# Performance work log

Hardware: AMD Instinct MI355X
Metric: run time of the kernel (lower is better)

The kernel has to match this reference:

```python
import jax, jax.numpy as jnp
import numpy as np
from jax import lax

# dims: batch, seq_len, d_model, heads, d_ff, num_scales, compression_ratio
B, L, D, H, F, S, CR = 4, 1024, 1024, 16, 4096, 4, 2


def setup_inputs() -> dict:
    key = jax.random.key(0)
    ks = jax.random.split(key, 12)
    def rn(k, shape, s=0.02):
        return jax.random.normal(k, shape, dtype=jnp.float32) * s
    return {
        'x': jax.random.normal(ks[0], (B, L, D), dtype=jnp.float32),
        'W_dc': rn(ks[1], (D, D, 3)),            # dilated conv kernel (OIH)
        'b_dc': jnp.zeros((D,), jnp.float32),
        'W_dec': rn(ks[2], (S - 1, D, D, CR)),    # strided decomposition convs
        'Wq': rn(ks[3], (S, D, D)),               # per-scale query proj
        'Wk': rn(ks[4], (S, D, D)),               # per-scale key proj
        'Wv': rn(ks[5], (D, D)),                  # shared value proj
        'Wo': rn(ks[6], (D, D)),                  # shared output proj
        'agg_logits': rn(ks[7], (S,), 1.0),       # convex aggregation logits
        'gamma1': jnp.ones((D,), jnp.float32), 'beta1': jnp.zeros((D,), jnp.float32),
        'gamma2': jnp.ones((D,), jnp.float32), 'beta2': jnp.zeros((D,), jnp.float32),
        'W1': rn(ks[8], (D, F)), 'b1': jnp.zeros((F,), jnp.float32),
        'W2': rn(ks[9], (F, D)), 'b2': jnp.zeros((D,), jnp.float32),
    }


def _conv1d(x_blc, w_oik, stride, pad, rdil):
    # x: [B, L, Cin] -> [B, L', Cout]; w: [Cout, Cin, K]
    y = lax.conv_general_dilated(
        x_blc.transpose(0, 2, 1), w_oik, (stride,), [(pad, pad)],
        rhs_dilation=(rdil,), dimension_numbers=('NCH', 'OIH', 'NCH'))
    return y.transpose(0, 2, 1)


def _ln(x, g, b, eps=1e-5):
    mu = x.mean(-1, keepdims=True)
    v = x.var(-1, keepdims=True)
    return (x - mu) * lax.rsqrt(v + eps) * g + b


def reference(x, W_dc, b_dc, W_dec, Wq, Wk, Wv, Wo, agg_logits,
              gamma1, beta1, gamma2, beta2, W1, b1, W2, b2):
    dh = D // H
    inv_sqrt_dh = 1.0 / jnp.sqrt(jnp.float32(dh))
    residual = x
    # 1. dilated conv (k=3, dil=2, pad=2 -> same length) + ReLU (dropout=eval/identity)
    xc = jax.nn.relu(_conv1d(x, W_dc, 1, 2, 2) + b_dc)
    # 2. hierarchical decomposition: strided convs halving seq length per scale
    scales = [xc]
    for s in range(S - 1):
        scales.append(_conv1d(scales[-1], W_dec[s], CR, 0, 1))
    # 3. multiscale attention: full-res queries attend to each compressed scale;
    #    value projection Wv shared across scales
    outs = []
    for s in range(S):
        Ls = scales[s].shape[1]
        q = (xc @ Wq[s]).reshape(B, L, H, dh)
        k = (scales[s] @ Wk[s]).reshape(B, Ls, H, dh)
        v = (scales[s] @ Wv).reshape(B, Ls, H, dh)
        att = jax.nn.softmax(jnp.einsum('bqhd,bkhd->bhqk', q, k) * inv_sqrt_dh, axis=-1)
        o = jnp.einsum('bhqk,bkhd->bqhd', att, v).reshape(B, L, D) @ Wo
        outs.append(o)
    # 4. convex (optimization-driven) aggregation + entropy sparsity aux loss
    w = jax.nn.softmax(agg_logits)
    maha = jnp.einsum('s,sbld->bld', w, jnp.stack(outs))
    aux_loss = -jnp.sum(w * jnp.log(w + 1e-9))
    # 5. residual + LN + FFN (exact GELU, as torch nn.GELU default)
    x1 = _ln(residual + maha, gamma1, beta1)
    ffn = jax.nn.gelu(x1 @ W1 + b1, approximate=False) @ W2 + b2
    out = _ln(x1 + ffn, gamma2, beta2)
    return out, aux_loss
```

## Files before the change

kernel.cpp:

```cpp
#include <hip/hip_runtime.h>
#include <cstddef>

#define DB 4
#define DL 1024
#define DD 1024
#define DH 16
#define DF 4096

typedef __attribute__((ext_vector_type(8))) short short8;
typedef __attribute__((ext_vector_type(4))) float float4v;

static __device__ __forceinline__ short f2bf(float f) {
    unsigned u = __float_as_uint(f);
    unsigned r = (u + 0x7FFFu + ((u >> 16) & 1u)) >> 16;
    return (short)r;
}

#define GLOAD_LDS16(gp, lp)                                                          \
    __builtin_amdgcn_global_load_lds(                                                \
        (const __attribute__((address_space(1))) void*)(gp),                         \
        (__attribute__((address_space(3))) void*)(lp), 16, 0, 0)

__global__ __launch_bounds__(256) void prep_all_kernel(
    const float* __restrict__ Wdc, const float* __restrict__ Wdec,
    const float* __restrict__ Wq, const float* __restrict__ Wk,
    const float* __restrict__ Wv, const float* __restrict__ Wo,
    const float* __restrict__ W1, const float* __restrict__ W2,
    const float* __restrict__ x, const float* __restrict__ agg,
    short* __restrict__ wdc_bt, short* __restrict__ wdec_bt,
    short* __restrict__ wq4t, short* __restrict__ wkvt, short* __restrict__ wot,
    short* __restrict__ w1t, short* __restrict__ w2t, short* __restrict__ xpad,
    float* __restrict__ wagg, float* __restrict__ aux) {
    __shared__ float tile[32][33];
    const size_t M1 = 1024 * 1024;
    int blk = blockIdx.x, tid = threadIdx.x;
    if (blk < 12288) {
        int idx = blk * 256 + tid;
        int i = idx & 1023, o = (idx >> 10) & 1023, k = idx >> 20;
        wdc_bt[idx] = f2bf(Wdc[((size_t)o * 1024 + i) * 3 + k]);
        return;
    }
    if (blk < 36864) {
        int idx = (blk - 12288) * 256 + tid;
        int i = idx & 1023, k2 = (idx >> 10) & 1, n = (idx >> 11) & 1023, s = idx >> 21;
        wdec_bt[idx] = f2bf(Wdec[(((size_t)(s * 1024 + n)) * 1024 + i) * 2 + k2]);
        return;
    }
    if (blk < 58368) {
        const float* src; short* dst; int K, N, bx, by;
        if (blk < 50176) {
            int r = blk - 36864;
            int z = r >> 10, rem = r & 1023;
            bx = rem & 31; by = rem >> 5; K = 1024; N = 1024;
            if (z < 4)      { src = Wq + (size_t)z * M1;       dst = wq4t + (size_t)z * M1; }
            else if (z < 8) { src = Wk + (size_t)(z - 4) * M1; dst = wkvt + (size_t)(z - 4) * 2 * M1; }
            else if (z < 12){ src = Wv;                        dst = wkvt + (size_t)(z - 8) * 2 * M1 + M1; }
            else            { src = Wo;                        dst = wot; }
        } else if (blk < 54272) {
            int r = blk - 50176;
            bx = r & 127; by = r >> 7; K = 1024; N = 4096; src = W1; dst = w1t;
        } else {
            int r = blk - 54272;
            bx = r & 31; by = r >> 5; K = 4096; N = 1024; src = W2; dst = w2t;
        }
        int n0 = bx << 5, k0 = by << 5;
        int cc = tid & 31, rr = tid >> 5;
#pragma unroll
        for (int p = 0; p < 4; p++) {
            int kk = (p << 3) + rr;
            tile[kk][cc] = src[(size_t)(k0 + kk) * N + n0 + cc];
        }
        __syncthreads();
#pragma unroll
        for (int p = 0; p < 4; p++) {
            int nn = (p << 3) + rr;
            dst[(size_t)(n0 + nn) * K + k0 + cc] = f2bf(tile[cc][nn]);
        }
        return;
    }
    if (blk < 74816) {
        int idx = (blk - 58368) * 256 + tid;
        int d = idx & 1023;
        int row = (idx >> 10) % 1028;
        int b = (idx >> 10) / 1028;
        int l = row - 2;
        float v = (l >= 0 && l < DL) ? x[((size_t)(b * DL + l)) * DD + d] : 0.f;
        xpad[idx] = f2bf(v);
        return;
    }
    if (tid == 0) {
        float l0 = agg[0], l1 = agg[1], l2 = agg[2], l3 = agg[3];
        float m = fmaxf(fmaxf(l0, l1), fmaxf(l2, l3));
        float e0 = __expf(l0 - m), e1 = __expf(l1 - m);
        float e2 = __expf(l2 - m), e3 = __expf(l3 - m);
        float ssum = e0 + e1 + e2 + e3;
        float w0 = e0 / ssum, w1 = e1 / ssum, w2 = e2 / ssum, w3 = e3 / ssum;
        wagg[0] = w0; wagg[1] = w1; wagg[2] = w2; wagg[3] = w3;
        *aux = -(w0 * logf(w0 + 1e-9f) + w1 * logf(w1 + 1e-9f) +
                 w2 * logf(w2 + 1e-9f) + w3 * logf(w3 + 1e-9f));
    }
}

template <int ACT, int OBF>
__global__ __launch_bounds__(256) void mgemm_kernel(
    const short* __restrict__ A, const short* __restrict__ Bt,
    const float* __restrict__ bias, void* __restrict__ Cv,
    int M, int N, int K) {
    __shared__ short As[128 * 32];
    __shared__ short Bs[128 * 32];
    int tid = threadIdx.x;
    int wave = tid >> 6, lane = tid & 63;
    int lq = lane & 15, quad = lane >> 4;
    int m0 = blockIdx.y << 7, n0 = blockIdx.x << 7;
    int wm = (wave & 1) << 6, wn = (wave >> 1) << 6;
    int r0 = tid >> 2, r1 = (256 + tid) >> 2;
    int kc0 = (tid & 3) << 3;
    const short* Ag0 = A + (size_t)(m0 + r0) * K + kc0;
    const short* Ag1 = A + (size_t)(m0 + r1) * K + kc0;
    const short* Bg0 = Bt + (size_t)(n0 + r0) * K + kc0;
    const short* Bg1 = Bt + (size_t)(n0 + r1) * K + kc0;
    float4v acc[4][4];
#pragma unroll
    for (int mi = 0; mi < 4; mi++)
#pragma unroll
        for (int ni = 0; ni < 4; ni++) acc[mi][ni] = (float4v){0.f, 0.f, 0.f, 0.f};

    for (int k0 = 0; k0 < K; k0 += 32) {
        __syncthreads();
        GLOAD_LDS16(Ag0 + k0, As + tid * 8);
        GLOAD_LDS16(Ag1 + k0, As + (256 + tid) * 8);
        GLOAD_LDS16(Bg0 + k0, Bs + tid * 8);
        GLOAD_LDS16(Bg1 + k0, Bs + (256 + tid) * 8);
        __syncthreads();
        short8 af[4], bfr[4];
#pragma unroll
        for (int mi = 0; mi < 4; mi++)
            af[mi] = *(const short8*)(As + ((wm + (mi << 4) + lq) << 5) + (quad << 3));
#pragma unroll
        for (int ni = 0; ni < 4; ni++)
            bfr[ni] = *(const short8*)(Bs + ((wn + (ni << 4) + lq) << 5) + (quad << 3));
#pragma unroll
        for (int mi = 0; mi < 4; mi++)
#pragma unroll
            for (int ni = 0; ni < 4; ni++)
                acc[mi][ni] = __builtin_amdgcn_mfma_f32_16x16x32_bf16(
                    af[mi], bfr[ni], acc[mi][ni], 0, 0, 0);
    }
#pragma unroll
    for (int ni = 0; ni < 4; ni++) {
        int col = n0 + wn + (ni << 4) + lq;
        float bv = bias ? bias[col] : 0.f;
#pragma unroll
        for (int mi = 0; mi < 4; mi++) {
#pragma unroll
            for (int r = 0; r < 4; r++) {
                int row = m0 + wm + (mi << 4) + (quad << 2) + r;
                float v = acc[mi][ni][r] + bv;
                if (ACT == 1) v = 0.5f * v * (1.0f + erff(v * 0.70710678118654752f));
                if (OBF) ((short*)Cv)[(size_t)row * N + col] = f2bf(v);
                else ((float*)Cv)[(size_t)row * N + col] = v;
            }
        }
    }
}

__global__ __launch_bounds__(256) void kvgemm_kernel(
    const short* __restrict__ acts, const short* __restrict__ wkvt,
    short* __restrict__ kvall, short* __restrict__ kfrall) {
    __shared__ short As[128 * 32];
    __shared__ short Bs[128 * 32];
    int my = blockIdx.y;
    int s = my < 32 ? 0 : my < 48 ? 1 : my < 56 ? 2 : 3;
    int m0 = my << 7;
    int rb = s == 0 ? 0 : s == 1 ? 4096 : s == 2 ? 6144 : 7168;
    size_t doff = s == 0 ? 0 : s == 1 ? 4194304 : s == 2 ? 6291456 : 7340032;
    int Ls = DL >> s;
    const short* Bt = wkvt + (size_t)s * 2097152;
    const int K = 1024, N = 2048;
    int tid = threadIdx.x;
    int wave = tid >> 6, lane = tid & 63;
    int lq = lane & 15, quad = lane >> 4;
    int n0 = blockIdx.x << 7;
    int wm = (wave & 1) << 6, wn = (wave >> 1) << 6;
    int r0 = tid >> 2, r1 = (256 + tid) >> 2;
    int kc0 = (tid & 3) << 3;
    const short* Ag0 = acts + (size_t)(m0 + r0) * K + kc0;
    const short* Ag1 = acts + (size_t)(m0 + r1) * K + kc0;
    const short* Bg0 = Bt + (size_t)(n0 + r0) * K + kc0;
    const short* Bg1 = Bt + (size_t)(n0 + r1) * K + kc0;
    float4v acc[4][4];
#pragma unroll
    for (int mi = 0; mi < 4; mi++)
#pragma unroll
        for (int ni = 0; ni < 4; ni++) acc[mi][ni] = (float4v){0.f, 0.f, 0.f, 0.f};
    for (int k0 = 0; k0 < K; k0 += 32) {
        __syncthreads();
        GLOAD_LDS16(Ag0 + k0, As + tid * 8);
        GLOAD_LDS16(Ag1 + k0, As + (256 + tid) * 8);
        GLOAD_LDS16(Bg0 + k0, Bs + tid * 8);
        GLOAD_LDS16(Bg1 + k0, Bs + (256 + tid) * 8);
        __syncthreads();
        short8 af[4], bfr[4];
#pragma unroll
        for (int mi = 0; mi < 4; mi++)
            af[mi] = *(const short8*)(As + ((wm + (mi << 4) + lq) << 5) + (quad << 3));
#pragma unroll
        for (int ni = 0; ni < 4; ni++)
            bfr[ni] = *(const short8*)(Bs + ((wn + (ni << 4) + lq) << 5) + (quad << 3));
#pragma unroll
        for (int mi = 0; mi < 4; mi++)
#pragma unroll
            for (int ni = 0; ni < 4; ni++)
                acc[mi][ni] = __builtin_amdgcn_mfma_f32_16x16x32_bf16(
                    af[mi], bfr[ni], acc[mi][ni], 0, 0, 0);
    }
    bool isK = (n0 < 1024);
#pragma unroll
    for (int ni = 0; ni < 4; ni++) {
        int col = n0 + wn + (ni << 4) + lq;
        if (isK) {
            int h = col >> 6, dc = (col >> 3) & 7, di = col & 7;
#pragma unroll
            for (int mi = 0; mi < 4; mi++)
#pragma unroll
                for (int r = 0; r < 4; r++) {
                    int row = m0 + wm + (mi << 4) + (quad << 2) + r;
                    int jg = row - rb;
                    int b = jg >> (10 - s);
                    int j = jg & (Ls - 1);
                    int bh = (b << 4) | h;
                    size_t addr = doff + (((size_t)bh * (Ls >> 4) + (j >> 4)) << 10) +
                                  (dc << 7) + ((j & 15) << 3) + di;
                    kfrall[addr] = f2bf(acc[mi][ni][r]);
                }
        } else {
#pragma unroll
            for (int mi = 0; mi < 4; mi++)
#pragma unroll
                for (int r = 0; r < 4; r++) {
                    int row = m0 + wm + (mi << 4) + (quad << 2) + r;
                    kvall[(size_t)row * N + col] = f2bf(acc[mi][ni][r]);
                }
        }
    }
}

__global__ __launch_bounds__(256) void mgemm_pk_kernel(
    const short* __restrict__ A, const short* __restrict__ Bt,
    const float* __restrict__ bias, float* __restrict__ Cout,
    int M, int N, int Kfull, int KH) {
    __shared__ short As[128 * 32];
    __shared__ short Bs[128 * 32];
    int kz = blockIdx.z;
    const short* Ab = A + (size_t)kz * KH;
    const short* Btb = Bt + (size_t)kz * KH;
    float* Co = Cout + (size_t)kz * M * N;
    int tid = threadIdx.x;
    int wave = tid >> 6, lane = tid & 63;
    int lq = lane & 15, quad = lane >> 4;
    int m0 = blockIdx.y << 7, n0 = blockIdx.x << 7;
    int wm = (wave & 1) << 6, wn = (wave >> 1) << 6;
    int r0 = tid >> 2, r1 = (256 + tid) >> 2;
    int kc0 = (tid & 3) << 3;
    const short* Ag0 = Ab + (size_t)(m0 + r0) * Kfull + kc0;
    const short* Ag1 = Ab + (size_t)(m0 + r1) * Kfull + kc0;
    const short* Bg0 = Btb + (size_t)(n0 + r0) * Kfull + kc0;
    const short* Bg1 = Btb + (size_t)(n0 + r1) * Kfull + kc0;
    float4v acc[4][4];
#pragma unroll
    for (int mi = 0; mi < 4; mi++)
#pragma unroll
        for (int ni = 0; ni < 4; ni++) acc[mi][ni] = (float4v){0.f, 0.f, 0.f, 0.f};
    for (int k0 = 0; k0 < KH; k0 += 32) {
        __syncthreads();
        GLOAD_LDS16(Ag0 + k0, As + tid * 8);
        GLOAD_LDS16(Ag1 + k0, As + (256 + tid) * 8);
        GLOAD_LDS16(Bg0 + k0, Bs + tid * 8);
        GLOAD_LDS16(Bg1 + k0, Bs + (256 + tid) * 8);
        __syncthreads();
        short8 af[4], bfr[4];
#pragma unroll
        for (int mi = 0; mi < 4; mi++)
            af[mi] = *(const short8*)(As + ((wm + (mi << 4) + lq) << 5) + (quad << 3));
#pragma unroll
        for (int ni = 0; ni < 4; ni++)
            bfr[ni] = *(const short8*)(Bs + ((wn + (ni << 4) + lq) << 5) + (quad << 3));
#pragma unroll
        for (int mi = 0; mi < 4; mi++)
#pragma unroll
            for (int ni = 0; ni < 4; ni++)
                acc[mi][ni] = __builtin_amdgcn_mfma_f32_16x16x32_bf16(
                    af[mi], bfr[ni], acc[mi][ni], 0, 0, 0);
    }
#pragma unroll
    for (int ni = 0; ni < 4; ni++) {
        int col = n0 + wn + (ni << 4) + lq;
        float bv = (bias && kz == 0) ? bias[col] : 0.f;
#pragma unroll
        for (int mi = 0; mi < 4; mi++)
#pragma unroll
            for (int r = 0; r < 4; r++) {
                int row = m0 + wm + (mi << 4) + (quad << 2) + r;
                __builtin_nontemporal_store(acc[mi][ni][r] + bv,
                                            &Co[(size_t)row * N + col]);
            }
    }
}

__global__ __launch_bounds__(256) void sumcast4_kernel(
    const float* __restrict__ p, size_t stride, short* __restrict__ outp) {
    int idx = (blockIdx.x * 256 + threadIdx.x) << 2;
    float4v a0 = __builtin_nontemporal_load((const float4v*)&p[idx]);
    float4v a1 = __builtin_nontemporal_load((const float4v*)&p[stride + idx]);
    float4v a2 = __builtin_nontemporal_load((const float4v*)&p[2 * stride + idx]);
    float4v a3 = __builtin_nontemporal_load((const float4v*)&p[3 * stride + idx]);
    ushort4 u;
    u.x = (unsigned short)f2bf(a0[0] + a1[0] + a2[0] + a3[0]);
    u.y = (unsigned short)f2bf(a0[1] + a1[1] + a2[1] + a3[1]);
    u.z = (unsigned short)f2bf(a0[2] + a1[2] + a2[2] + a3[2]);
    u.w = (unsigned short)f2bf(a0[3] + a1[3] + a2[3] + a3[3]);
    *(ushort4*)&outp[idx] = u;
}

__global__ __launch_bounds__(256) void convdil_pk_kernel(
    const short* __restrict__ xp, const short* __restrict__ Wt,
    float* __restrict__ pbuf) {
    __shared__ short As[128 * 32];
    __shared__ short Bs[128 * 32];
    int kp = blockIdx.z;
    int tid = threadIdx.x;
    int wave = tid >> 6, lane = tid & 63;
    int lq = lane & 15, quad = lane >> 4;
    int m0 = blockIdx.y << 7, n0 = blockIdx.x << 7;
    int wm = (wave & 1) << 6, wn = (wave >> 1) << 6;
    int b = m0 >> 10, ll0 = m0 & 1023;
    int r0 = tid >> 2, r1 = (256 + tid) >> 2;
    int kc = (tid & 3) << 3;
    float* Co = pbuf + (size_t)kp * DB * DL * DD;
    const short* Abase = xp + ((size_t)(b * 1028 + ll0 + 2 * kp)) * DD + kc;
    const short* Bbase = Wt + (size_t)kp * DD * DD;
    const short* Bg0 = Bbase + (size_t)(n0 + r0) * DD + kc;
    const short* Bg1 = Bbase + (size_t)(n0 + r1) * DD + kc;
    float4v acc[4][4];
#pragma unroll
    for (int mi = 0; mi < 4; mi++)
#pragma unroll
        for (int ni = 0; ni < 4; ni++) acc[mi][ni] = (float4v){0.f, 0.f, 0.f, 0.f};
    for (int k0 = 0; k0 < DD; k0 += 32) {
        __syncthreads();
        GLOAD_LDS16(Abase + (size_t)r0 * DD + k0, As + tid * 8);
        GLOAD_LDS16(Abase + (size_t)r1 * DD + k0, As + (256 + tid) * 8);
        GLOAD_LDS16(Bg0 + k0, Bs + tid * 8);
        GLOAD_LDS16(Bg1 + k0, Bs + (256 + tid) * 8);
        __syncthreads();
        short8 af[4], bfr[4];
#pragma unroll
        for (int mi = 0; mi < 4; mi++)
            af[mi] = *(const short8*)(As + ((wm + (mi << 4) + lq) << 5) + (quad << 3));
#pragma unroll
        for (int ni = 0; ni < 4; ni++)
            bfr[ni] = *(const short8*)(Bs + ((wn + (ni << 4) + lq) << 5) + (quad << 3));
#pragma unroll
        for (int mi = 0; mi < 4; mi++)
#pragma unroll
            for (int ni = 0; ni < 4; ni++)
                acc[mi][ni] = __builtin_amdgcn_mfma_f32_16x16x32_bf16(
                    af[mi], bfr[ni], acc[mi][ni], 0, 0, 0);
    }
#pragma unroll
    for (int ni = 0; ni < 4; ni++) {
        int col = n0 + wn + (ni << 4) + lq;
#pragma unroll
        for (int mi = 0; mi < 4; mi++)
#pragma unroll
            for (int r = 0; r < 4; r++) {
                int row = m0 + wm + (mi << 4) + (quad << 2) + r;
                __builtin_nontemporal_store(acc[mi][ni][r],
                                            &Co[(size_t)row * DD + col]);
            }
    }
}

__global__ __launch_bounds__(256) void convcomb_kernel(
    const float* __restrict__ pbuf, const float* __restrict__ bvec,
    short* __restrict__ xcb) {
    const size_t M4 = (size_t)DB * DL * DD;
    int idx = (blockIdx.x * 256 + threadIdx.x) << 2;
    int col = idx & 1023;
    float4v p0 = __builtin_nontemporal_load((const float4v*)&pbuf[idx]);
    float4v p1 = __builtin_nontemporal_load((const float4v*)&pbuf[M4 + idx]);
    float4v p2 = __builtin_nontemporal_load((const float4v*)&pbuf[2 * M4 + idx]);
    float4v bb = *(const float4v*)&bvec[col];
    ushort4 u;
    u.x = (unsigned short)f2bf(fmaxf(p0[0] + p1[0] + p2[0] + bb[0], 0.f));
    u.y = (unsigned short)f2bf(fmaxf(p0[1] + p1[1] + p2[1] + bb[1], 0.f));
    u.z = (unsigned short)f2bf(fmaxf(p0[2] + p1[2] + p2[2] + bb[2], 0.f));
    u.w = (unsigned short)f2bf(fmaxf(p0[3] + p1[3] + p2[3] + bb[3], 0.f));
    *(ushort4*)&xcb[idx] = u;
}

__global__ __launch_bounds__(256) void vfrag_all_kernel(const short* __restrict__ kvall,
                                                        short* __restrict__ vfr0) {
    __shared__ short tile[32][33];
    int flat = blockIdx.x;
    int s, base, rb;
    size_t doff;
    if (flat < 4096)      { s = 0; base = 0;    rb = 0;    doff = 0; }
    else if (flat < 6144) { s = 1; base = 4096; rb = 4096; doff = 4194304; }
    else if (flat < 7168) { s = 2; base = 6144; rb = 6144; doff = 6291456; }
    else                  { s = 3; base = 7168; rb = 7168; doff = 7340032; }
    int rem = flat - base;
    int Ls = DL >> s;
    int nt = Ls >> 5;
    int j0t = rem & (nt - 1);
    int rest = rem >> (5 - s);
    int dt = rest & 1;
    int bh = rest >> 1;
    int j0 = j0t << 5, d0 = dt << 5;
    int b = bh >> 4, h = bh & 15;
    int tid = threadIdx.x;
    int cc = tid & 31, rr = tid >> 5;
#pragma unroll
    for (int p = 0; p < 4; p++) {
        int jj = (p << 3) + rr;
        tile[jj][cc] = kvall[((size_t)(rb + b * Ls + j0 + jj) << 11) + 1024 +
                             (h << 6) + d0 + cc];
    }
    __syncthreads();
    int c = j0 >> 6, ks = (j0 >> 5) & 1;
    int pc = (((cc >> 2) & 1) << 4) | ((cc >> 3) << 2) | (cc & 3);
#pragma unroll
    for (int p = 0; p < 4; p++) {
        int d = d0 + (p << 3) + rr;
        int tt = d >> 4, lqv = d & 15;
        size_t off = doff + (((size_t)bh * (Ls >> 6) + c) << 12) + (ks << 11) +
                     (tt << 9) + (lqv << 5) + cc;
        vfr0[off] = tile[pc][(p << 3) + rr];
    }
}

static __device__ __forceinline__ float fexp2(float x) {
    return __builtin_amdgcn_exp2f(x);
}

#define LOADK(DST, TILE)                                                          \
    {                                                                             \
        int _ti = (TILE);                                                         \
        _Pragma("unroll") for (int t = 0; t < 4; t++) {                           \
            const short* _kp = kfb + ((size_t)((_ti << 2) + t) << 10);            \
            DST[2 * t] = *(const short8*)_kp;                                     \
            DST[2 * t + 1] = *(const short8*)(_kp + 512);                         \
        }                                                                         \
    }

#define LOADV(DST, TILE)                                                          \
    {                                                                             \
        const short* _vcb = vfb + ((size_t)(TILE) << 12);                         \
        _Pragma("unroll") for (int ks = 0; ks < 2; ks++)                          \
            _Pragma("unroll") for (int t = 0; t < 4; t++)                         \
                DST[ks * 4 + t] = *(const short8*)(_vcb + (ks << 11) + (t << 9)); \
    }

#define ATTN_STEP(KF, VF)                                                         \
    {                                                                             \
        float4v S[4];                                                             \
        _Pragma("unroll") for (int t = 0; t < 4; t++) {                           \
            float4v zz = (float4v){0.f, 0.f, 0.f, 0.f};                           \
            zz = __builtin_amdgcn_mfma_f32_16x16x32_bf16(KF[2 * t], qf0, zz, 0, 0, 0); \
            S[t] = __builtin_amdgcn_mfma_f32_16x16x32_bf16(KF[2 * t + 1], qf1, zz, 0, 0, 0); \
        }                                                                         \
        unsigned wpk[8];                                                          \
        _Pragma("unroll") for (int t = 0; t < 4; t++) {                           \
            float p0 = fexp2(S[t][0] * c_exp);                                    \
            float p1 = fexp2(S[t][1] * c_exp);                                    \
            float p2 = fexp2(S[t][2] * c_exp);                                    \
            float p3 = fexp2(S[t][3] * c_exp);                                    \
            lsum += p0 + p1 + p2 + p3;                                            \
            wpk[2 * t] = (__float_as_uint(p1) & 0xFFFF0000u) |                    \
                         (__float_as_uint(p0) >> 16);                             \
            wpk[2 * t + 1] = (__float_as_uint(p3) & 0xFFFF0000u) |                \
                             (__float_as_uint(p2) >> 16);                         \
        }                                                                         \
        union AFU { unsigned u[4]; short8 s8; };                                  \
        AFU af0, af1;                                                             \
        af0.u[0] = wpk[0]; af0.u[1] = wpk[1]; af0.u[2] = wpk[2]; af0.u[3] = wpk[3]; \
        af1.u[0] = wpk[4]; af1.u[1] = wpk[5]; af1.u[2] = wpk[6]; af1.u[3] = wpk[7]; \
        _Pragma("unroll") for (int t = 0; t < 4; t++)                             \
            O[t] = __builtin_amdgcn_mfma_f32_16x16x32_bf16(af0.s8, VF[t], O[t], 0, 0, 0); \
        _Pragma("unroll") for (int t = 0; t < 4; t++)                             \
            O[t] = __builtin_amdgcn_mfma_f32_16x16x32_bf16(af1.s8, VF[4 + t], O[t], 0, 0, 0); \
    }

__global__ __launch_bounds__(256) void attn_fused8_kernel(
    const short* __restrict__ qb4, const short* __restrict__ kfr0,
    const short* __restrict__ vfr0, const float* __restrict__ wagg,
    short* __restrict__ attb) {
    int tid = threadIdx.x;
    int w = tid >> 6, lane = tid & 63;
    int lq = lane & 15, quad = lane >> 4;
    int bh = blockIdx.x;
    int b = bh >> 4, h = bh & 15;
    int qrow0 = b * DL + (blockIdx.y << 6) + (w << 4);
    const float c_exp = 0.18033688f;

    float fin[4][4];
#pragma unroll
    for (int t = 0; t < 4; t++)
#pragma unroll
        for (int r = 0; r < 4; r++) fin[t][r] = 0.f;

#pragma unroll 1
    for (int s = 0; s < 4; s++) {
        int Ls = DL >> s;
        size_t doff = s == 0 ? 0 : s == 1 ? 4194304 : s == 2 ? 6291456 : 7340032;

        const short* qbase = qb4 + ((size_t)(qrow0 + lq) << 12) + (s << 10) +
                             (h << 6) + (quad << 3);
        short8 qf0 = __builtin_nontemporal_load((const short8*)qbase);
        short8 qf1 = __builtin_nontemporal_load((const short8*)(qbase + 32));

        const short* kfb = kfr0 + doff + (((size_t)bh * (Ls >> 4)) << 10) +
                           (quad << 7) + (lq << 3);
        const short* vfb = vfr0 + doff + (((size_t)bh * (Ls >> 6)) << 12) +
                           (lq << 5) + (quad << 3);

        float4v O[4];
        float lsum = 0.f;
#pragma unroll
        for (int t = 0; t < 4; t++) O[t] = (float4v){0.f, 0.f, 0.f, 0.f};

        short8 kA[8], kB[8], vA[8], vB[8];
        int nt = Ls >> 6;
        LOADK(kA, 0);
#pragma unroll 1
        for (int c = 0; c < nt; c += 2) {
            LOADV(vA, c);
            LOADK(kB, c + 1);
            ATTN_STEP(kA, vA);
            LOADV(vB, c + 1);
            { int nx = (c + 2 < nt) ? c + 2 : 0; LOADK(kA, nx); }
            ATTN_STEP(kB, vB);
        }

        lsum += __shfl_xor(lsum, 16, 64);
        lsum += __shfl_xor(lsum, 32, 64);
        float wsc = wagg[s];
#pragma unroll
        for (int r = 0; r < 4; r++) {
            int sl = (lane & 48) | (((lane >> 4) << 2) + r);
            float lr = __shfl(lsum, sl, 64);
            float linv = wsc / lr;
#pragma unroll
            for (int t = 0; t < 4; t++) fin[t][r] += O[t][r] * linv;
        }
    }
#pragma unroll
    for (int r = 0; r < 4; r++) {
        size_t rbase = ((size_t)(qrow0 + (quad << 2) + r) << 10) + (h << 6) + lq;
#pragma unroll
        for (int t = 0; t < 4; t++)
            attb[rbase + (t << 4)] = f2bf(fin[t][r]);
    }
}

template <int NP, int OBF>
__global__ __launch_bounds__(256) void addlnN_kernel(
    const float* __restrict__ a, const float* __restrict__ pb, size_t pstride,
    const float* __restrict__ gam, const float* __restrict__ bet,
    float* __restrict__ out, short* __restrict__ outb) {
    __shared__ float redA[4], redB[4];
    int row = blockIdx.x, tid = threadIdx.x;
    size_t base = (size_t)row * DD + (tid << 2);
    float4v av = *(const float4v*)&a[base];
    float s0 = av[0], s1 = av[1], s2 = av[2], s3 = av[3];
#pragma unroll
    for (int j = 0; j < NP; j++) {
        float4v pv = __builtin_nontemporal_load(
            (const float4v*)&pb[(size_t)j * pstride + base]);
        s0 += pv[0]; s1 += pv[1]; s2 += pv[2]; s3 += pv[3];
    }
    float lsum = s0 + s1 + s2 + s3;
    float lsq = s0 * s0 + s1 * s1 + s2 * s2 + s3 * s3;
#pragma unroll
    for (int o = 32; o > 0; o >>= 1) {
        lsum += __shfl_down(lsum, o, 64);
        lsq += __shfl_down(lsq, o, 64);
    }
    int lane = tid & 63, wid = tid >> 6;
    if (lane == 0) { redA[wid] = lsum; redB[wid] = lsq; }
    __syncthreads();
    float tsum = redA[0] + redA[1] + redA[2] + redA[3];
    float tsq = redB[0] + redB[1] + redB[2] + redB[3];
    float mean = tsum * (1.0f / DD);
    float var = tsq * (1.0f / DD) - mean * mean;
    float rstd = rsqrtf(var + 1e-5f);
    float4v gv = *(const float4v*)&gam[tid << 2];
    float4v bev = *(const float4v*)&bet[tid << 2];
    float4v o;
    o[0] = (s0 - mean) * rstd * gv[0] + bev[0];
    o[1] = (s1 - mean) * rstd * gv[1] + bev[1];
    o[2] = (s2 - mean) * rstd * gv[2] + bev[2];
    o[3] = (s3 - mean) * rstd * gv[3] + bev[3];
    *(float4v*)&out[base] = o;
    if (OBF) {
        ushort4 u;
        u.x = (unsigned short)f2bf(o[0]);
        u.y = (unsigned short)f2bf(o[1]);
        u.z = (unsigned short)f2bf(o[2]);
        u.w = (unsigned short)f2bf(o[3]);
        *(ushort4*)&outb[base] = u;
    }
}

extern "C" void kernel_launch(void* const* d_in, const int* in_sizes, int n_in,
                              void* d_out, int out_size, void* d_ws, size_t ws_size,
                              hipStream_t stream) {
    (void)in_sizes; (void)n_in; (void)out_size; (void)ws_size;
    const float* x   = (const float*)d_in[0];
    const float* Wdc = (const float*)d_in[1];
    const float* bdc = (const float*)d_in[2];
    const float* Wdec= (const float*)d_in[3];
    const float* Wq  = (const float*)d_in[4];
    const float* Wk  = (const float*)d_in[5];
    const float* Wv  = (const float*)d_in[6];
    const float* Wo  = (const float*)d_in[7];
    const float* agg = (const float*)d_in[8];
    const float* g1  = (const float*)d_in[9];
    const float* be1 = (const float*)d_in[10];
    const float* g2  = (const float*)d_in[11];
    const float* be2 = (const float*)d_in[12];
    const float* W1  = (const float*)d_in[13];
    const float* b1  = (const float*)d_in[14];
    const float* W2  = (const float*)d_in[15];
    const float* b2  = (const float*)d_in[16];
    float* out = (float*)d_out;

    float* ws = (float*)d_ws;
    size_t off = 0;
    auto alloc = [&](size_t nfloats) { float* p = ws + off; off += nfloats; return p; };
    const size_t M1 = 1024 * 1024;
    short* wdc_bt  = (short*)alloc(3 * M1 / 2);
    short* wdec_bt = (short*)alloc(3 * M1);
    short* wq4t    = (short*)alloc(2 * M1);
    short* wkvt    = (short*)alloc(4 * M1);
    short* wot     = (short*)alloc(M1 / 2);
    short* w1t     = (short*)alloc(2 * M1);
    short* w2t     = (short*)alloc(2 * M1);
    float* wagg    = alloc(64);
    short* xpad    = (short*)alloc(2105344);
    short* xcb     = (short*)alloc(2 * M1);
    short* s1b     = (short*)alloc(M1);
    short* s2b     = (short*)alloc(M1 / 2);
    short* s3b     = (short*)alloc(M1 / 4);
    short* qb4     = (short*)alloc(8 * M1);
    short* kvall   = (short*)alloc(7 * M1 + M1 / 2);
    short* kfrall  = (short*)alloc(3 * M1 + 3 * M1 / 4);
    short* vfrall  = (short*)alloc(3 * M1 + 3 * M1 / 4);
    short* attb    = (short*)alloc(2 * M1);
    float* x1      = alloc(4 * M1);
    short* x1b     = (short*)alloc(2 * M1);
    float* pkbuf   = alloc(8 * M1);
    short* hb      = qb4;
    float* convp   = (float*)qb4;
    float* pk4     = (float*)kvall;

    dim3 blk(256);
    prep_all_kernel<<<dim3(74817), blk, 0, stream>>>(
        Wdc, Wdec, Wq, Wk, Wv, Wo, W1, W2, x, agg,
        wdc_bt, wdec_bt, wq4t, wkvt, wot, w1t, w2t, xpad, wagg,
        out + (size_t)DB * DL * DD);

    convdil_pk_kernel<<<dim3(DD / 128, DB * DL / 128, 3), blk, 0, stream>>>(
        xpad, wdc_bt, convp);
    convcomb_kernel<<<dim3(4 * M1 / (256 * 4)), blk, 0, stream>>>(convp, bdc, xcb);

    mgemm_pk_kernel<<<dim3(8, 16, 4), blk, 0, stream>>>(
        xcb, wdec_bt, nullptr, pkbuf, 2048, DD, 2 * DD, 512);
    sumcast4_kernel<<<dim3(2 * M1 / 1024), blk, 0, stream>>>(pkbuf, 2 * M1, s1b);
    mgemm_pk_kernel<<<dim3(8, 8, 4), blk, 0, stream>>>(
        s1b, wdec_bt + 2 * M1, nullptr, pkbuf, 1024, DD, 2 * DD, 512);
    sumcast4_kernel<<<dim3(M1 / 1024), blk, 0, stream>>>(pkbuf, M1, s2b);
    mgemm_pk_kernel<<<dim3(8, 4, 4), blk, 0, stream>>>(
        s2b, wdec_bt + 4 * M1, nullptr, pkbuf, 512, DD, 2 * DD, 512);
    sumcast4_kernel<<<dim3(M1 / 2048), blk, 0, stream>>>(pkbuf, M1 / 2, s3b);

    mgemm_kernel<0, 1><<<dim3(32, 32), blk, 0, stream>>>(
        xcb, wq4t, nullptr, qb4, DB * DL, 4 * DD, DD);

    kvgemm_kernel<<<dim3(16, 60), blk, 0, stream>>>(xcb, wkvt, kvall, kfrall);

    vfrag_all_kernel<<<dim3(7680), blk, 0, stream>>>(kvall, vfrall);

    attn_fused8_kernel<<<dim3(DB * DH, DL / 64), blk, 0, stream>>>(
        qb4, kfrall, vfrall, wagg, attb);

    mgemm_pk_kernel<<<dim3(8, 32, 2), blk, 0, stream>>>(
        attb, wot, nullptr, pkbuf, DB * DL, DD, DD, DD / 2);

    addlnN_kernel<2, 1><<<dim3(DB * DL), blk, 0, stream>>>(
        x, pkbuf, 4 * M1, g1, be1, x1, x1b);

    mgemm_kernel<1, 1><<<dim3(DF / 128, (DB * DL) / 128), blk, 0, stream>>>(
        x1b, w1t, b1, hb, DB * DL, DF, DD);
    mgemm_pk_kernel<<<dim3(8, 32, 4), blk, 0, stream>>>(
        hb, w2t, b2, pk4, DB * DL, DD, DF, DF / 4);

    addlnN_kernel<4, 0><<<dim3(DB * DL), blk, 0, stream>>>(
        x1, pk4, 4 * M1, g2, be2, out, nullptr);
}
```

Before: 729.5 us.

## Stage K/V fragments through double-buffered LDS with async global-to-LDS loads

The attention kernel stops having each of the four waves load its own K and V fragments from global memory into registers. Instead the block cooperatively copies each 64-key tile into a double-buffered shared-memory area using global_load_lds and reads the fragments back from LDS. The V fragment layout written by vfrag_all_kernel is permuted to match the new LDS read pattern. This cuts redundant global/L2 traffic (each wave reads the same K/V) and register pressure, at the cost of a __syncthreads per tile and 32KB of LDS per block.

```diff
diff --git a/kernel.cpp b/kernel.cpp
--- a/kernel.cpp
+++ b/kernel.cpp
@@ -434,7 +434,7 @@
         int d = d0 + (p << 3) + rr;
         int tt = d >> 4, lqv = d & 15;
         size_t off = doff + (((size_t)bh * (Ls >> 6) + c) << 12) + (ks << 11) +
-                     (tt << 9) + (lqv << 5) + cc;
+                     (tt << 9) + ((cc & 24) << 4) + (lqv << 3) + (cc & 7);
         vfr0[off] = tile[pc][(p << 3) + rr];
     }
 }
@@ -443,58 +443,21 @@
     return __builtin_amdgcn_exp2f(x);
 }
 
-#define LOADK(DST, TILE)                                                          \
+#define STAGE9(BUF, TILE)                                                         \
     {                                                                             \
-        int _ti = (TILE);                                                         \
-        _Pragma("unroll") for (int t = 0; t < 4; t++) {                           \
-            const short* _kp = kfb + ((size_t)((_ti << 2) + t) << 10);            \
-            DST[2 * t] = *(const short8*)_kp;                                     \
-            DST[2 * t + 1] = *(const short8*)(_kp + 512);                         \
-        }                                                                         \
-    }
-
-#define LOADV(DST, TILE)                                                          \
-    {                                                                             \
-        const short* _vcb = vfb + ((size_t)(TILE) << 12);                         \
-        _Pragma("unroll") for (int ks = 0; ks < 2; ks++)                          \
-            _Pragma("unroll") for (int t = 0; t < 4; t++)                         \
-                DST[ks * 4 + t] = *(const short8*)(_vcb + (ks << 11) + (t << 9)); \
-    }
-
-#define ATTN_STEP(KF, VF)                                                         \
-    {                                                                             \
-        float4v S[4];                                                             \
-        _Pragma("unroll") for (int t = 0; t < 4; t++) {                           \
-            float4v zz = (float4v){0.f, 0.f, 0.f, 0.f};                           \
-            zz = __builtin_amdgcn_mfma_f32_16x16x32_bf16(KF[2 * t], qf0, zz, 0, 0, 0); \
-            S[t] = __builtin_amdgcn_mfma_f32_16x16x32_bf16(KF[2 * t + 1], qf1, zz, 0, 0, 0); \
-        }                                                                         \
-        unsigned wpk[8];                                                          \
-        _Pragma("unroll") for (int t = 0; t < 4; t++) {                           \
-            float p0 = fexp2(S[t][0] * c_exp);                                    \
-            float p1 = fexp2(S[t][1] * c_exp);                                    \
-            float p2 = fexp2(S[t][2] * c_exp);                                    \
-            float p3 = fexp2(S[t][3] * c_exp);                                    \
-            lsum += p0 + p1 + p2 + p3;                                            \
-            wpk[2 * t] = (__float_as_uint(p1) & 0xFFFF0000u) |                    \
-                         (__float_as_uint(p0) >> 16);                             \
-            wpk[2 * t + 1] = (__float_as_uint(p3) & 0xFFFF0000u) |                \
-                             (__float_as_uint(p2) >> 16);                         \
-        }                                                                         \
-        union AFU { unsigned u[4]; short8 s8; };                                  \
-        AFU af0, af1;                                                             \
-        af0.u[0] = wpk[0]; af0.u[1] = wpk[1]; af0.u[2] = wpk[2]; af0.u[3] = wpk[3]; \
-        af1.u[0] = wpk[4]; af1.u[1] = wpk[5]; af1.u[2] = wpk[6]; af1.u[3] = wpk[7]; \
-        _Pragma("unroll") for (int t = 0; t < 4; t++)                             \
-            O[t] = __builtin_amdgcn_mfma_f32_16x16x32_bf16(af0.s8, VF[t], O[t], 0, 0, 0); \
-        _Pragma("unroll") for (int t = 0; t < 4; t++)                             \
-            O[t] = __builtin_amdgcn_mfma_f32_16x16x32_bf16(af1.s8, VF[4 + t], O[t], 0, 0, 0); \
-    }
-
-__global__ __launch_bounds__(256) void attn_fused8_kernel(
+        const short* _gs = (w < 2)                                                \
+            ? kt + ((size_t)(TILE) << 12) + (w << 11) + (lane << 3)               \
+            : vt + ((size_t)(TILE) << 12) + ((w - 2) << 11) + (lane << 3);        \
+        short* _lb = sbuf[BUF] + (w << 11) + (lane << 3);                         \
+        _Pragma("unroll") for (int _i = 0; _i < 4; _i++)                          \
+            GLOAD_LDS16(_gs + (_i << 9), _lb + (_i << 9));                        \
+    }
+
+__global__ __launch_bounds__(256) void attn_fused9_kernel(
     const short* __restrict__ qb4, const short* __restrict__ kfr0,
     const short* __restrict__ vfr0, const float* __restrict__ wagg,
     short* __restrict__ attb) {
+    __shared__ __align__(16) short sbuf[2][8192];
     int tid = threadIdx.x;
     int w = tid >> 6, lane = tid & 63;
     int lq = lane & 15, quad = lane >> 4;
@@ -502,6 +465,7 @@
     int b = bh >> 4, h = bh & 15;
     int qrow0 = b * DL + (blockIdx.y << 6) + (w << 4);
     const float c_exp = 0.18033688f;
+    int fo = (quad << 7) + (lq << 3);
 
     float fin[4][4];
 #pragma unroll
@@ -519,28 +483,63 @@
         short8 qf0 = __builtin_nontemporal_load((const short8*)qbase);
         short8 qf1 = __builtin_nontemporal_load((const short8*)(qbase + 32));
 
-        const short* kfb = kfr0 + doff + (((size_t)bh * (Ls >> 4)) << 10) +
-                           (quad << 7) + (lq << 3);
-        const short* vfb = vfr0 + doff + (((size_t)bh * (Ls >> 6)) << 12) +
-                           (lq << 5) + (quad << 3);
+        const short* kt = kfr0 + doff + (((size_t)bh * (Ls >> 4)) << 10);
+        const short* vt = vfr0 + doff + (((size_t)bh * (Ls >> 6)) << 12);
 
         float4v O[4];
         float lsum = 0.f;
 #pragma unroll
         for (int t = 0; t < 4; t++) O[t] = (float4v){0.f, 0.f, 0.f, 0.f};
 
-        short8 kA[8], kB[8], vA[8], vB[8];
         int nt = Ls >> 6;
-        LOADK(kA, 0);
+        STAGE9(0, 0);
 #pragma unroll 1
-        for (int c = 0; c < nt; c += 2) {
-            LOADV(vA, c);
-            LOADK(kB, c + 1);
-            ATTN_STEP(kA, vA);
-            LOADV(vB, c + 1);
-            { int nx = (c + 2 < nt) ? c + 2 : 0; LOADK(kA, nx); }
-            ATTN_STEP(kB, vB);
+        for (int c = 0; c < nt; c++) {
+            __syncthreads();
+            int cur = c & 1;
+            if (c + 1 < nt) STAGE9(cur ^ 1, c + 1);
+            const short* kl = sbuf[cur] + fo;
+            const short* vl = sbuf[cur] + 4096 + fo;
+
+            float4v S[4];
+#pragma unroll
+            for (int t = 0; t < 4; t++) {
+                short8 kf0 = *(const short8*)(kl + (t << 10));
+                short8 kf1 = *(const short8*)(kl + (t << 10) + 512);
+                float4v zz = (float4v){0.f, 0.f, 0.f, 0.f};
+                zz = __builtin_amdgcn_mfma_f32_16x16x32_bf16(kf0, qf0, zz, 0, 0, 0);
+                S[t] = __builtin_amdgcn_mfma_f32_16x16x32_bf16(kf1, qf1, zz, 0, 0, 0);
+            }
+
+            unsigned wpk[8];
+#pragma unroll
+            for (int t = 0; t < 4; t++) {
+                float p0 = fexp2(S[t][0] * c_exp);
+                float p1 = fexp2(S[t][1] * c_exp);
+                float p2 = fexp2(S[t][2] * c_exp);
+                float p3 = fexp2(S[t][3] * c_exp);
+                lsum += p0 + p1 + p2 + p3;
+                wpk[2 * t]     = (__float_as_uint(p1) & 0xFFFF0000u) |
+                                 (__float_as_uint(p0) >> 16);
+                wpk[2 * t + 1] = (__float_as_uint(p3) & 0xFFFF0000u) |
+                                 (__float_as_uint(p2) >> 16);
+            }
+            union AFU { unsigned u[4]; short8 s8; };
+            AFU af0, af1;
+            af0.u[0] = wpk[0]; af0.u[1] = wpk[1]; af0.u[2] = wpk[2]; af0.u[3] = wpk[3];
+            af1.u[0] = wpk[4]; af1.u[1] = wpk[5]; af1.u[2] = wpk[6]; af1.u[3] = wpk[7];
+#pragma unroll
+            for (int t = 0; t < 4; t++) {
+                short8 vf = *(const short8*)(vl + (t << 9));
+                O[t] = __builtin_amdgcn_mfma_f32_16x16x32_bf16(af0.s8, vf, O[t], 0, 0, 0);
+            }
+#pragma unroll
+            for (int t = 0; t < 4; t++) {
+                short8 vf = *(const short8*)(vl + 2048 + (t << 9));
+                O[t] = __builtin_amdgcn_mfma_f32_16x16x32_bf16(af1.s8, vf, O[t], 0, 0, 0);
+            }
         }
+        __syncthreads();
 
         lsum += __shfl_xor(lsum, 16, 64);
         lsum += __shfl_xor(lsum, 32, 64);
@@ -691,7 +690,7 @@
 
     vfrag_all_kernel<<<dim3(7680), blk, 0, stream>>>(kvall, vfrall);
 
-    attn_fused8_kernel<<<dim3(DB * DH, DL / 64), blk, 0, stream>>>(
+    attn_fused9_kernel<<<dim3(DB * DH, DL / 64), blk, 0, stream>>>(
         qb4, kfrall, vfrall, wagg, attb);
 
     mgemm_pk_kernel<<<dim3(8, 32, 2), blk, 0, stream>>>(
```

Result: faster. 700.8 us (-3.9%).
